# Kernel optimization log

Measured on AMD Instinct MI355X. Metric: run time of the kernel, lower is better.

## Reference

```python
import jax, jax.numpy as jnp
import numpy as np

EMBED_DIM = 1024
NUM_HEADS = 16
HEAD_DIM = EMBED_DIM // NUM_HEADS


def setup_inputs() -> dict:
    key = jax.random.key(0)
    ks = jax.random.split(key, 7)
    B, S, E = 8, 1024, EMBED_DIM
    # xavier-uniform-like scale for in_proj_weight [3E, E]
    bound_in = float(np.sqrt(6.0 / (3 * E + E)))
    bound_out = float(np.sqrt(6.0 / (E + E)))
    return {
        "q": jax.random.normal(ks[0], (B, S, E), jnp.float32),
        "k": jax.random.normal(ks[1], (B, S, E), jnp.float32),
        "v": jax.random.normal(ks[2], (B, S, E), jnp.float32),
        "in_proj_weight": jax.random.uniform(ks[3], (3 * E, E), jnp.float32, -bound_in, bound_in),
        "in_proj_bias": jnp.zeros((3 * E,), jnp.float32),
        "out_proj_weight": jax.random.uniform(ks[4], (E, E), jnp.float32, -bound_out, bound_out),
        "out_proj_bias": jnp.zeros((E,), jnp.float32),
    }


def reference(q, k, v, in_proj_weight, in_proj_bias, out_proj_weight, out_proj_bias):
    B, S, E = q.shape
    H, D = NUM_HEADS, HEAD_DIM
    w_q, w_k, w_v = jnp.split(in_proj_weight, 3, axis=0)
    b_q, b_k, b_v = jnp.split(in_proj_bias, 3, axis=0)
    # packed in-projection: linear(x, W, b) = x @ W.T + b
    qp = q @ w_q.T + b_q
    kp = k @ w_k.T + b_k
    vp = v @ w_v.T + b_v
    # [B, S, E] -> [B, H, S, D]
    qh = qp.reshape(B, S, H, D).transpose(0, 2, 1, 3)
    kh = kp.reshape(B, S, H, D).transpose(0, 2, 1, 3)
    vh = vp.reshape(B, S, H, D).transpose(0, 2, 1, 3)
    scale = D ** -0.5
    # explicit full attention in fp32 (matches original fp32 cast path)
    scores = jnp.einsum("bhqd,bhkd->bhqk", qh, kh) * scale
    attn = jax.nn.softmax(scores, axis=-1)
    ctx = jnp.einsum("bhqk,bhkd->bhqd", attn, vh)  # [B, H, S, D]
    ctx = ctx.transpose(0, 2, 1, 3).reshape(B, S, E)
    out = ctx @ out_proj_weight.T + out_proj_bias
    return out
```

## Files before the change

### kernel.cpp

```cpp
#include <hip/hip_runtime.h>
#include <stdint.h>

#define TOK 8192
#define EDIM 1024
#define NH 16
#define HD 64
#define SEQ 1024
#define BATCH 8

typedef short bf16x8 __attribute__((ext_vector_type(8)));
typedef short bf16x4 __attribute__((ext_vector_type(4)));
typedef float f32x4 __attribute__((ext_vector_type(4)));
typedef float f32x16 __attribute__((ext_vector_type(16)));
typedef unsigned int u32x2 __attribute__((ext_vector_type(2)));
typedef unsigned int u32x4 __attribute__((ext_vector_type(4)));

__device__ __forceinline__ short f2bf(float f) {
  union { float f; uint32_t u; } c; c.f = f;
  uint32_t u = c.u;
  u += 0x7FFFu + ((u >> 16) & 1u);
  return (short)(u >> 16);
}
__device__ __forceinline__ float bf2f(short h) {
  union { uint32_t u; float f; } c; c.u = ((uint32_t)(uint16_t)h) << 16;
  return c.f;
}
__device__ __forceinline__ uint32_t bfr(float f) {
  union { float f; uint32_t u; } c; c.f = f;
  return (c.u + 0x8000u) >> 16;
}
__device__ __forceinline__ uint32_t cvtpk(float lo, float hi_) {
  uint32_t r;
  asm("v_cvt_pk_bf16_f32 %0, %1, %2" : "=v"(r) : "v"(lo), "v"(hi_));
  return r;
}

#define GLDS16(ldsp, gp) __builtin_amdgcn_global_load_lds( \
    (__attribute__((address_space(1))) void*)(gp),          \
    (__attribute__((address_space(3))) void*)(ldsp), 16, 0, 0)

__global__ __launch_bounds__(256) void cast_all(
    const float* __restrict__ q, const float* __restrict__ k,
    const float* __restrict__ v, const float* __restrict__ wi,
    const float* __restrict__ wo, short* __restrict__ dst) {
  const size_t NTOK = (size_t)TOK * EDIM;
  const size_t NWI = 3u * EDIM * EDIM;
  size_t i = ((size_t)blockIdx.x * 256 + threadIdx.x) * 4;
  const float* src;
  if (i < NTOK) src = q + i;
  else if (i < 2 * NTOK) src = k + (i - NTOK);
  else if (i < 3 * NTOK) src = v + (i - 2 * NTOK);
  else if (i < 3 * NTOK + NWI) src = wi + (i - 3 * NTOK);
  else src = wo + (i - 3 * NTOK - NWI);
  float4 f = *(const float4*)src;
  bf16x4 o;
  o[0] = f2bf(f.x); o[1] = f2bf(f.y); o[2] = f2bf(f.z); o[3] = f2bf(f.w);
  *(bf16x4*)(dst + i) = o;
}

#define GEMM_TILE(KT, VMC, DOSTAGE)                                            \
  {                                                                            \
    asm volatile("s_waitcnt vmcnt(" VMC ")" ::: "memory");                     \
    __builtin_amdgcn_s_barrier();                                              \
    const int buf_ = (KT) & 3;                                                 \
    const short* Ab = lds + buf_ * 16384;                                      \
    const short* Bb = Ab + 8192;                                               \
    bf16x8 af[8], bv[4];                                                       \
    _Pragma("unroll")                                                          \
    for (int mi = 0; mi < 4; mi++)                                             \
      af[mi] = *(const bf16x8*)&Ab[(wrBase + mi * 16 + fr) * 32 + fg * 8];     \
    _Pragma("unroll")                                                          \
    for (int ni = 0; ni < 4; ni++)                                             \
      bv[ni] = *(const bf16x8*)&Bb[(wcBase + ni * 16 + fr) * 32 + fg * 8];     \
    if (DOSTAGE) {                                                             \
      char* d_ = (char*)lds + (((KT) + 3) & 3) * 32768 + t * 16;               \
      GLDS16(d_, aS + ((KT) + 3) * 32);                                        \
      GLDS16(d_ + 8192, aS + ((KT) + 3) * 32 + 128 * 1024);                    \
    }                                                                          \
    __builtin_amdgcn_s_setprio(1);                                             \
    _Pragma("unroll")                                                          \
    for (int mi = 0; mi < 4; mi++) {                                           \
      _Pragma("unroll")                                                        \
      for (int ni = 0; ni < 4; ni++)                                           \
        acc[mi][ni] = __builtin_amdgcn_mfma_f32_16x16x32_bf16(                 \
            af[mi], bv[ni], acc[mi][ni], 0, 0, 0);                             \
    }                                                                          \
    __builtin_amdgcn_s_setprio(0);                                             \
    _Pragma("unroll")                                                          \
    for (int mi = 4; mi < 8; mi++)                                             \
      af[mi] = *(const bf16x8*)&Ab[(wrBase + mi * 16 + fr) * 32 + fg * 8];     \
    if (DOSTAGE) {                                                             \
      char* d_ = (char*)lds + (((KT) + 3) & 3) * 32768 + 16384 + t * 16;       \
      GLDS16(d_, bS + ((KT) + 3) * 32);                                        \
      GLDS16(d_ + 8192, bS + ((KT) + 3) * 32 + 128 * 1024);                    \
    }                                                                          \
    __builtin_amdgcn_s_barrier();                                              \
    __builtin_amdgcn_s_setprio(1);                                             \
    _Pragma("unroll")                                                          \
    for (int mi = 4; mi < 8; mi++) {                                           \
      _Pragma("unroll")                                                        \
      for (int ni = 0; ni < 4; ni++)                                           \
        acc[mi][ni] = __builtin_amdgcn_mfma_f32_16x16x32_bf16(                 \
            af[mi], bv[ni], acc[mi][ni], 0, 0, 0);                             \
    }                                                                          \
    __builtin_amdgcn_s_setprio(0);                                             \
  }

template<int MODE>
__global__ __launch_bounds__(512, 1)
void gemm_bt8(const short* __restrict__ Abase, const short* __restrict__ Wbase,
              const float* __restrict__ biasBase, void* __restrict__ outv) {
  __shared__ short lds[65536];

  const int z = (MODE == 0) ? blockIdx.z : 0;
  const size_t NTOK = (size_t)TOK * EDIM;
  const short* A  = Abase + (size_t)z * NTOK;
  const short* Bw = Wbase + (size_t)z * EDIM * EDIM;
  const float* bias = biasBase + z * EDIM;

  const int t = threadIdx.x;
  const int l = t & 63, w = t >> 6;
  const int fr = l & 15, fg = l >> 4;
  const int wrBase = (w >> 2) * 128;
  const int wcBase = (w & 3) * 64;
  const int rowBase = blockIdx.x * 256;
  const int colBase = blockIdx.y * 256;

  f32x4 acc[8][4];
#pragma unroll
  for (int i = 0; i < 8; i++)
#pragma unroll
    for (int j = 0; j < 4; j++) acc[i][j] = (f32x4){0.f, 0.f, 0.f, 0.f};

  const short* aS = A  + (size_t)(rowBase + (t >> 2)) * EDIM + (t & 3) * 8;
  const short* bS = Bw + (size_t)(colBase + (t >> 2)) * EDIM + (t & 3) * 8;

#pragma unroll
  for (int s = 0; s < 3; s++) {
    char* d = (char*)lds + s * 32768 + t * 16;
    GLDS16(d,         aS + s * 32);
    GLDS16(d + 8192,  aS + s * 32 + 128 * 1024);
    GLDS16(d + 16384, bS + s * 32);
    GLDS16(d + 24576, bS + s * 32 + 128 * 1024);
  }

#pragma unroll 1
  for (int kt = 0; kt < 30; kt++) {
    GEMM_TILE(kt, "8", (kt <= 28));
  }
  GEMM_TILE(30, "4", false);
  GEMM_TILE(31, "0", false);

#pragma unroll
  for (int mi = 0; mi < 8; mi++)
#pragma unroll
    for (int ni = 0; ni < 4; ni++)
#pragma unroll
      for (int r = 0; r < 4; r++) {
        int grow = rowBase + wrBase + mi * 16 + fg * 4 + r;
        int gcol = colBase + wcBase + ni * 16 + fr;
        float v = acc[mi][ni][r] + bias[gcol];
        if (MODE == 0) {
          int b_ = grow >> 10, s_ = grow & 1023;
          int h_ = gcol >> 6,  d_ = gcol & 63;
          short* outp = (short*)outv + (size_t)z * NTOK;
          outp[((size_t)((b_ * NH + h_) * SEQ + s_) << 6) | d_] = f2bf(v);
        } else {
          ((float*)outv)[(size_t)grow * EDIM + gcol] = v;
        }
      }
}

__global__ __launch_bounds__(512)
void attn_fwd7(const short* __restrict__ proj, short* __restrict__ ctx) {
  __shared__ short lds[16384];

  const int t = threadIdx.x;
  const int l = t & 63, w = t >> 6;
  const int ln = l & 31, hi = l >> 5;

  const int n = blockIdx.x + 4 * (blockIdx.y + 16 * blockIdx.z);
  const int qt = (n >> 3) & 3;
  const int hl = (n & 7) | ((n >> 5) << 3);
  const int h = hl & 15, b = hl >> 4;

  const size_t NTOK = (size_t)TOK * EDIM;
  const size_t headOff = (size_t)(b * NH + h) * SEQ * HD;
  const short* Qp = proj + headOff;
  const short* Kp = proj + NTOK + headOff;
  const short* Vp = proj + 2 * NTOK + headOff;

  const int q0 = qt * 256;
  const int qrow = q0 + w * 32 + ln;

  const int kRow = t >> 3;
  const int kCol = ((t & 7) ^ (kRow & 7)) << 3;
  const int vd0  = w * 8;

  const float qscale = 0.18033688011112042f;
  bf16x8 bQ[4];
#pragma unroll
  for (int ds = 0; ds < 4; ds++) {
    bf16x8 v = *(const bf16x8*)(Qp + (size_t)qrow * HD + ds * 16 + hi * 8);
#pragma unroll
    for (int j = 0; j < 8; j++) v[j] = (short)bfr(bf2f(v[j]) * qscale);
    bQ[ds] = v;
  }

  float m_run = -3.0e38f;
  float l_acc[4] = {0.f, 0.f, 0.f, 0.f};
  f32x16 ot[2];
#pragma unroll
  for (int i = 0; i < 16; i++) { ot[0][i] = 0.f; ot[1][i] = 0.f; }

  {
    GLDS16((char*)lds + t * 16, Kp + (size_t)kRow * HD + kCol);
    bf16x8 v0 = *(const bf16x8*)(Vp + (size_t)l * HD + vd0);
    char* VtB = (char*)lds + 8192;
#pragma unroll
    for (int jj = 0; jj < 8; jj++) {
      int d = vd0 + jj;
      *(short*)(VtB + d * 128 + (((l >> 3) ^ (d & 7)) << 4) + (l & 7) * 2) = v0[jj];
    }
  }
  __syncthreads();

  for (int jt = 0; jt < SEQ / 64; jt++) {
    const int bufByte = (jt & 1) << 14;
    const int nb = bufByte ^ (1 << 14);
    const bool have_next = (jt + 1 < SEQ / 64);

    bf16x8 nv0;
    if (have_next) {
      const int kv1 = (jt + 1) * 64;
      GLDS16((char*)lds + nb + t * 16, Kp + (size_t)(kv1 + kRow) * HD + kCol);
      nv0 = *(const bf16x8*)(Vp + (size_t)(kv1 + l) * HD + vd0);
    }

    f32x16 sa[2];
#pragma unroll
    for (int i = 0; i < 16; i++) { sa[0][i] = 0.f; sa[1][i] = 0.f; }
    __builtin_amdgcn_s_setprio(1);
#pragma unroll
    for (int ds = 0; ds < 4; ds++) {
#pragma unroll
      for (int kvb = 0; kvb < 2; kvb++) {
        int kv = kvb * 32 + ln;
        bf16x8 aK = *(const bf16x8*)((const char*)lds + bufByte + kv * 128 +
                                     (((ds * 2 + hi) ^ (kv & 7)) << 4));
        sa[kvb] = __builtin_amdgcn_mfma_f32_32x32x16_bf16(aK, bQ[ds], sa[kvb], 0, 0, 0);
      }
    }
    __builtin_amdgcn_s_setprio(0);

    float tr[11];
#pragma unroll
    for (int j = 0; j < 10; j++) {
      float a = (3 * j + 0 < 16) ? sa[0][3 * j + 0] : sa[1][3 * j - 16];
      float b2 = (3 * j + 1 < 16) ? sa[0][3 * j + 1] : sa[1][3 * j - 15];
      float c = (3 * j + 2 < 16) ? sa[0][3 * j + 2] : sa[1][3 * j - 14];
      tr[j] = fmaxf(fmaxf(a, b2), c);
    }
    tr[10] = fmaxf(sa[1][14], sa[1][15]);
    float u0 = fmaxf(fmaxf(tr[0], tr[1]), tr[2]);
    float u1 = fmaxf(fmaxf(tr[3], tr[4]), tr[5]);
    float u2 = fmaxf(fmaxf(tr[6], tr[7]), tr[8]);
    float u3 = fmaxf(tr[9], tr[10]);
    float vmax = fmaxf(fmaxf(fmaxf(u0, u1), u2), u3);
    vmax = fmaxf(vmax, __shfl_xor(vmax, 32));

    int grow = !__all(vmax <= m_run + 8.0f);
    float alpha = 1.0f;
    if (grow) {
      float m_new = fmaxf(m_run, vmax);
      alpha = exp2f(m_run - m_new);
      m_run = m_new;
    }
    float ps[4] = {0.f, 0.f, 0.f, 0.f};
#pragma unroll
    for (int i = 0; i < 16; i++) {
      float p0 = exp2f(sa[0][i] - m_run);
      float p1 = exp2f(sa[1][i] - m_run);
      sa[0][i] = p0; sa[1][i] = p1;
      ps[i & 3] += p0 + p1;
    }
#pragma unroll
    for (int j = 0; j < 4; j++) l_acc[j] = l_acc[j] * alpha + ps[j];

    bf16x8 pa[4];
#pragma unroll
    for (int ks = 0; ks < 4; ks++) {
      const int kvb = ks >> 1, hf = (ks & 1) * 8;
      uint32_t A1 = cvtpk(sa[kvb][hf + 0], sa[kvb][hf + 1]);
      uint32_t A2 = cvtpk(sa[kvb][hf + 2], sa[kvb][hf + 3]);
      uint32_t B1 = cvtpk(sa[kvb][hf + 4], sa[kvb][hf + 5]);
      uint32_t B2 = cvtpk(sa[kvb][hf + 6], sa[kvb][hf + 7]);
      u32x4 wds;
#if __has_builtin(__builtin_amdgcn_permlane32_swap)
      u32x2 r13 = __builtin_amdgcn_permlane32_swap(A1, B1, false, false);
      u32x2 r24 = __builtin_amdgcn_permlane32_swap(A2, B2, false, false);
      wds[0] = r13[0]; wds[2] = r13[1];
      wds[1] = r24[0]; wds[3] = r24[1];
#else
      uint32_t send1 = hi ? A1 : B1;
      uint32_t send2 = hi ? A2 : B2;
      uint32_t recv1 = (uint32_t)__shfl_xor((int)send1, 32);
      uint32_t recv2 = (uint32_t)__shfl_xor((int)send2, 32);
      wds[0] = hi ? recv1 : A1;
      wds[1] = hi ? recv2 : A2;
      wds[2] = hi ? B1 : recv1;
      wds[3] = hi ? B2 : recv2;
#endif
      pa[ks] = __builtin_bit_cast(bf16x8, wds);
    }

    if (grow) {
#pragma unroll
      for (int i = 0; i < 16; i++) { ot[0][i] *= alpha; ot[1][i] *= alpha; }
    }
    const char* VtB = (const char*)lds + bufByte + 8192;
    __builtin_amdgcn_s_setprio(1);
#pragma unroll
    for (int ks = 0; ks < 4; ks++) {
#pragma unroll
      for (int dblk = 0; dblk < 2; dblk++) {
        int d = dblk * 32 + ln;
        bf16x8 aV = *(const bf16x8*)(VtB + d * 128 + (((ks * 2 + hi) ^ (d & 7)) << 4));
        ot[dblk] = __builtin_amdgcn_mfma_f32_32x32x16_bf16(aV, pa[ks], ot[dblk], 0, 0, 0);
      }
    }
    __builtin_amdgcn_s_setprio(0);

    if (have_next) {
      char* VtN = (char*)lds + nb + 8192;
#pragma unroll
      for (int jj = 0; jj < 8; jj++) {
        int d = vd0 + jj;
        *(short*)(VtN + d * 128 + (((l >> 3) ^ (d & 7)) << 4) + (l & 7) * 2) = nv0[jj];
      }
    }

    __syncthreads();
  }

  float l_run = (l_acc[0] + l_acc[1]) + (l_acc[2] + l_acc[3]);
  l_run += __shfl_xor(l_run, 32);
  float rl = 1.0f / l_run;

#pragma unroll
  for (int dblk = 0; dblk < 2; dblk++)
#pragma unroll
    for (int r = 0; r < 16; r++) {
      int d = dblk * 32 + (r & 3) + 8 * (r >> 2) + 4 * hi;
      int qrl = w * 32 + ln;
      int byteoff = qrl * 128 + (((d >> 3) ^ (qrl & 7)) << 4) + (d & 7) * 2;
      *(short*)((char*)lds + byteoff) = (short)bfr(ot[dblk][r] * rl);
    }
  __syncthreads();
#pragma unroll
  for (int i = 0; i < 4; i++) {
    int chunk = t * 4 + i;
    int row = chunk >> 3, c8 = chunk & 7;
    bf16x8 vv = *(const bf16x8*)((const char*)lds + row * 128 + ((c8 ^ (row & 7)) << 4));
    *(bf16x8*)(ctx + (size_t)(b * SEQ + q0 + row) * EDIM + h * HD + c8 * 8) = vv;
  }
}

extern "C" void kernel_launch(void* const* d_in, const int* in_sizes, int n_in,
                              void* d_out, int out_size, void* d_ws, size_t ws_size,
                              hipStream_t stream) {
  const float* q  = (const float*)d_in[0];
  const float* k  = (const float*)d_in[1];
  const float* v  = (const float*)d_in[2];
  const float* wi = (const float*)d_in[3];
  const float* bi = (const float*)d_in[4];
  const float* wo = (const float*)d_in[5];
  const float* bo = (const float*)d_in[6];
  float* out = (float*)d_out;

  short* ws = (short*)d_ws;
  const size_t NTOK = (size_t)TOK * EDIM;
  short* qkv_bf   = ws;
  short* w_in_bf  = qkv_bf + 3 * NTOK;
  short* w_out_bf = w_in_bf + 3 * (size_t)EDIM * EDIM;
  short* proj_bf  = w_out_bf + (size_t)EDIM * EDIM;
  short* ctx_bf   = qkv_bf;

  const size_t totalCast = 3 * NTOK + 3 * (size_t)EDIM * EDIM + (size_t)EDIM * EDIM;
  cast_all<<<dim3((unsigned)(totalCast / 4 / 256)), 256, 0, stream>>>(q, k, v, wi, wo, qkv_bf);

  gemm_bt8<0><<<dim3(TOK / 256, EDIM / 256, 3), 512, 0, stream>>>(qkv_bf, w_in_bf, bi, proj_bf);
  attn_fwd7<<<dim3(SEQ / 256, NH, BATCH), 512, 0, stream>>>(proj_bf, ctx_bf);
  gemm_bt8<1><<<dim3(TOK / 256, EDIM / 256, 1), 512, 0, stream>>>(ctx_bf, w_out_bf, bo, out);
}
```

Before: 190.2 us.

## Software-pipeline QK^T of next tile with softmax of current tile in attention

Restructures the attention loop so the QK^T MFMAs for tile jt+1 are computed while the softmax exponentials and bf16 packing for tile jt run, with score registers ping-ponging between two sets. K/V staging in LDS goes from a double buffer to a four-slot ring (64 KB), with global loads issued two tiles ahead. The aim is to overlap MFMA work with VALU/transcendental work and hide load latency. The costs are more registers and twice the LDS, which may lower occupancy.

```diff
diff --git a/kernel.cpp b/kernel.cpp
--- a/kernel.cpp
+++ b/kernel.cpp
@@ -172,8 +172,8 @@
 }
 
 __global__ __launch_bounds__(512)
-void attn_fwd7(const short* __restrict__ proj, short* __restrict__ ctx) {
-  __shared__ short lds[16384];
+void attn_fwd8(const short* __restrict__ proj, short* __restrict__ ctx) {
+  __shared__ short lds[32768];
 
   const int t = threadIdx.x;
   const int l = t & 63, w = t >> 6;
@@ -213,139 +213,186 @@
 #pragma unroll
   for (int i = 0; i < 16; i++) { ot[0][i] = 0.f; ot[1][i] = 0.f; }
 
+  f32x16 saA[2], saB[2];
+  bf16x8 nvA, nvB;
+
   {
-    GLDS16((char*)lds + t * 16, Kp + (size_t)kRow * HD + kCol);
-    bf16x8 v0 = *(const bf16x8*)(Vp + (size_t)l * HD + vd0);
-    char* VtB = (char*)lds + 8192;
+    GLDS16((char*)lds + t * 16,         Kp + (size_t)kRow * HD + kCol);
+    GLDS16((char*)lds + 16384 + t * 16, Kp + (size_t)(64 + kRow) * HD + kCol);
+    bf16x8 v0r = *(const bf16x8*)(Vp + (size_t)l * HD + vd0);
+    nvB = *(const bf16x8*)(Vp + (size_t)(64 + l) * HD + vd0);
+    char* Vt0 = (char*)lds + 8192;
 #pragma unroll
     for (int jj = 0; jj < 8; jj++) {
       int d = vd0 + jj;
-      *(short*)(VtB + d * 128 + (((l >> 3) ^ (d & 7)) << 4) + (l & 7) * 2) = v0[jj];
+      *(short*)(Vt0 + d * 128 + (((l >> 3) ^ (d & 7)) << 4) + (l & 7) * 2) = v0r[jj];
     }
-  }
-  __syncthreads();
-
-  for (int jt = 0; jt < SEQ / 64; jt++) {
-    const int bufByte = (jt & 1) << 14;
-    const int nb = bufByte ^ (1 << 14);
-    const bool have_next = (jt + 1 < SEQ / 64);
-
-    bf16x8 nv0;
-    if (have_next) {
-      const int kv1 = (jt + 1) * 64;
-      GLDS16((char*)lds + nb + t * 16, Kp + (size_t)(kv1 + kRow) * HD + kCol);
-      nv0 = *(const bf16x8*)(Vp + (size_t)(kv1 + l) * HD + vd0);
+    __syncthreads();
+#pragma unroll
+    for (int kvb = 0; kvb < 2; kvb++) {
+      f32x16 s = {};
+#pragma unroll
+      for (int ds = 0; ds < 4; ds++) {
+        int kv = kvb * 32 + ln;
+        bf16x8 aK = *(const bf16x8*)((const char*)lds + kv * 128 +
+                                     (((ds * 2 + hi) ^ (kv & 7)) << 4));
+        s = __builtin_amdgcn_mfma_f32_32x32x16_bf16(aK, bQ[ds], s, 0, 0, 0);
+      }
+      saA[kvb] = s;
     }
-
-    f32x16 sa[2];
-#pragma unroll
-    for (int i = 0; i < 16; i++) { sa[0][i] = 0.f; sa[1][i] = 0.f; }
-    __builtin_amdgcn_s_setprio(1);
-#pragma unroll
-    for (int ds = 0; ds < 4; ds++) {
-#pragma unroll
-      for (int kvb = 0; kvb < 2; kvb++) {
-        int kv = kvb * 32 + ln;
-        bf16x8 aK = *(const bf16x8*)((const char*)lds + bufByte + kv * 128 +
-                                     (((ds * 2 + hi) ^ (kv & 7)) << 4));
-        sa[kvb] = __builtin_amdgcn_mfma_f32_32x32x16_bf16(aK, bQ[ds], sa[kvb], 0, 0, 0);
-      }
-    }
-    __builtin_amdgcn_s_setprio(0);
-
-    float tr[11];
-#pragma unroll
-    for (int j = 0; j < 10; j++) {
-      float a = (3 * j + 0 < 16) ? sa[0][3 * j + 0] : sa[1][3 * j - 16];
-      float b2 = (3 * j + 1 < 16) ? sa[0][3 * j + 1] : sa[1][3 * j - 15];
-      float c = (3 * j + 2 < 16) ? sa[0][3 * j + 2] : sa[1][3 * j - 14];
-      tr[j] = fmaxf(fmaxf(a, b2), c);
-    }
-    tr[10] = fmaxf(sa[1][14], sa[1][15]);
-    float u0 = fmaxf(fmaxf(tr[0], tr[1]), tr[2]);
-    float u1 = fmaxf(fmaxf(tr[3], tr[4]), tr[5]);
-    float u2 = fmaxf(fmaxf(tr[6], tr[7]), tr[8]);
-    float u3 = fmaxf(tr[9], tr[10]);
-    float vmax = fmaxf(fmaxf(fmaxf(u0, u1), u2), u3);
-    vmax = fmaxf(vmax, __shfl_xor(vmax, 32));
-
-    int grow = !__all(vmax <= m_run + 8.0f);
-    float alpha = 1.0f;
-    if (grow) {
-      float m_new = fmaxf(m_run, vmax);
-      alpha = exp2f(m_run - m_new);
-      m_run = m_new;
-    }
-    float ps[4] = {0.f, 0.f, 0.f, 0.f};
-#pragma unroll
-    for (int i = 0; i < 16; i++) {
-      float p0 = exp2f(sa[0][i] - m_run);
-      float p1 = exp2f(sa[1][i] - m_run);
-      sa[0][i] = p0; sa[1][i] = p1;
-      ps[i & 3] += p0 + p1;
-    }
-#pragma unroll
-    for (int j = 0; j < 4; j++) l_acc[j] = l_acc[j] * alpha + ps[j];
-
-    bf16x8 pa[4];
-#pragma unroll
-    for (int ks = 0; ks < 4; ks++) {
-      const int kvb = ks >> 1, hf = (ks & 1) * 8;
-      uint32_t A1 = cvtpk(sa[kvb][hf + 0], sa[kvb][hf + 1]);
-      uint32_t A2 = cvtpk(sa[kvb][hf + 2], sa[kvb][hf + 3]);
-      uint32_t B1 = cvtpk(sa[kvb][hf + 4], sa[kvb][hf + 5]);
-      uint32_t B2 = cvtpk(sa[kvb][hf + 6], sa[kvb][hf + 7]);
-      u32x4 wds;
-#if __has_builtin(__builtin_amdgcn_permlane32_swap)
-      u32x2 r13 = __builtin_amdgcn_permlane32_swap(A1, B1, false, false);
-      u32x2 r24 = __builtin_amdgcn_permlane32_swap(A2, B2, false, false);
-      wds[0] = r13[0]; wds[2] = r13[1];
-      wds[1] = r24[0]; wds[3] = r24[1];
-#else
-      uint32_t send1 = hi ? A1 : B1;
-      uint32_t send2 = hi ? A2 : B2;
-      uint32_t recv1 = (uint32_t)__shfl_xor((int)send1, 32);
-      uint32_t recv2 = (uint32_t)__shfl_xor((int)send2, 32);
-      wds[0] = hi ? recv1 : A1;
-      wds[1] = hi ? recv2 : A2;
-      wds[2] = hi ? B1 : recv1;
-      wds[3] = hi ? B2 : recv2;
-#endif
-      pa[ks] = __builtin_bit_cast(bf16x8, wds);
-    }
-
-    if (grow) {
-#pragma unroll
-      for (int i = 0; i < 16; i++) { ot[0][i] *= alpha; ot[1][i] *= alpha; }
-    }
-    const char* VtB = (const char*)lds + bufByte + 8192;
-    __builtin_amdgcn_s_setprio(1);
-#pragma unroll
-    for (int ks = 0; ks < 4; ks++) {
-#pragma unroll
-      for (int dblk = 0; dblk < 2; dblk++) {
-        int d = dblk * 32 + ln;
-        bf16x8 aV = *(const bf16x8*)(VtB + d * 128 + (((ks * 2 + hi) ^ (d & 7)) << 4));
-        ot[dblk] = __builtin_amdgcn_mfma_f32_32x32x16_bf16(aV, pa[ks], ot[dblk], 0, 0, 0);
-      }
-    }
-    __builtin_amdgcn_s_setprio(0);
-
-    if (have_next) {
-      char* VtN = (char*)lds + nb + 8192;
-#pragma unroll
-      for (int jj = 0; jj < 8; jj++) {
-        int d = vd0 + jj;
-        *(short*)(VtN + d * 128 + (((l >> 3) ^ (d & 7)) << 4) + (l & 7) * 2) = nv0[jj];
-      }
-    }
-
-    __syncthreads();
-  }
+  }
+
+#define ATTN_BODY(JT, SACUR, SANEXT, NVOLD, NVNEW)                             \
+  {                                                                            \
+    const int jt_ = (JT);                                                      \
+    __syncthreads();             \
+    if (jt_ + 2 < 16) {                       \
+      const int kv2 = (jt_ + 2) * 64;                                          \
+      GLDS16((char*)lds + ((jt_ + 2) & 3) * 16384 + t * 16,                    \
+             Kp + (size_t)(kv2 + kRow) * HD + kCol);                           \
+      NVNEW = *(const bf16x8*)(Vp + (size_t)(kv2 + l) * HD + vd0);             \
+    }                                                                          \
+                                                      \
+    float tr[11];                                                              \
+    _Pragma("unroll")                                                          \
+    for (int j = 0; j < 10; j++) {                                             \
+      float a_ = (3 * j + 0 < 16) ? SACUR[0][3 * j + 0] : SACUR[1][3 * j - 16];\
+      float b_ = (3 * j + 1 < 16) ? SACUR[0][3 * j + 1] : SACUR[1][3 * j - 15];\
+      float c_ = (3 * j + 2 < 16) ? SACUR[0][3 * j + 2] : SACUR[1][3 * j - 14];\
+      tr[j] = fmaxf(fmaxf(a_, b_), c_);                                        \
+    }                                                                          \
+    tr[10] = fmaxf(SACUR[1][14], SACUR[1][15]);                                \
+    float u0 = fmaxf(fmaxf(tr[0], tr[1]), tr[2]);                              \
+    float u1 = fmaxf(fmaxf(tr[3], tr[4]), tr[5]);                              \
+    float u2 = fmaxf(fmaxf(tr[6], tr[7]), tr[8]);                              \
+    float vmax = fmaxf(fmaxf(fmaxf(u0, u1), u2), fmaxf(tr[9], tr[10]));        \
+    vmax = fmaxf(vmax, __shfl_xor(vmax, 32));                                  \
+    int grow = !__all(vmax <= m_run + 8.0f);                                   \
+    float alpha = 1.0f;                                                        \
+    if (grow) {                                                                \
+      float m_new = fmaxf(m_run, vmax);                                        \
+      alpha = exp2f(m_run - m_new);                                            \
+      m_run = m_new;                                                           \
+    }                                                                          \
+    float ps[4] = {0.f, 0.f, 0.f, 0.f};                                        \
+    bf16x8 pa[4];                                                              \
+                 \
+    {                                                                          \
+      float p[16];                                                             \
+      _Pragma("unroll")                                                        \
+      for (int i = 0; i < 16; i++) {                                           \
+        p[i] = exp2f(SACUR[0][i] - m_run);                                     \
+        ps[i & 3] += p[i];                                                     \
+      }                                                                        \
+      _Pragma("unroll")                                                        \
+      for (int ks = 0; ks < 2; ks++) {                                         \
+        const int hf = ks * 8;                                                 \
+        uint32_t A1 = cvtpk(p[hf + 0], p[hf + 1]);                             \
+        uint32_t A2 = cvtpk(p[hf + 2], p[hf + 3]);                             \
+        uint32_t B1 = cvtpk(p[hf + 4], p[hf + 5]);                             \
+        uint32_t B2 = cvtpk(p[hf + 6], p[hf + 7]);                             \
+        u32x4 wds;                                                             \
+        u32x2 r13 = __builtin_amdgcn_permlane32_swap(A1, B1, false, false);    \
+        u32x2 r24 = __builtin_amdgcn_permlane32_swap(A2, B2, false, false);    \
+        wds[0] = r13[0]; wds[2] = r13[1];                                      \
+        wds[1] = r24[0]; wds[3] = r24[1];                                      \
+        pa[ks] = __builtin_bit_cast(bf16x8, wds);                              \
+      }                                                                        \
+    }                                                                          \
+    if (jt_ + 1 < 16) {      \
+      f32x16 s = {};                                                           \
+      _Pragma("unroll")                                                        \
+      for (int ds = 0; ds < 4; ds++) {                                         \
+        int kv = ln;                                                           \
+        bf16x8 aK = *(const bf16x8*)((const char*)lds +                        \
+                     ((jt_ + 1) & 3) * 16384 + kv * 128 +                      \
+                     (((ds * 2 + hi) ^ (kv & 7)) << 4));                       \
+        s = __builtin_amdgcn_mfma_f32_32x32x16_bf16(aK, bQ[ds], s, 0, 0, 0);   \
+      }                                                                        \
+      SANEXT[0] = s;                                                           \
+    }                                                                          \
+                                                                   \
+    {                                                                          \
+      float p[16];                                                             \
+      _Pragma("unroll")                                                        \
+      for (int i = 0; i < 16; i++) {                                           \
+        p[i] = exp2f(SACUR[1][i] - m_run);                                     \
+        ps[i & 3] += p[i];                                                     \
+      }                                                                        \
+      _Pragma("unroll")                                                        \
+      for (int ks = 0; ks < 2; ks++) {                                         \
+        const int hf = ks * 8;                                                 \
+        uint32_t A1 = cvtpk(p[hf + 0], p[hf + 1]);                             \
+        uint32_t A2 = cvtpk(p[hf + 2], p[hf + 3]);                             \
+        uint32_t B1 = cvtpk(p[hf + 4], p[hf + 5]);                             \
+        uint32_t B2 = cvtpk(p[hf + 6], p[hf + 7]);                             \
+        u32x4 wds;                                                             \
+        u32x2 r13 = __builtin_amdgcn_permlane32_swap(A1, B1, false, false);    \
+        u32x2 r24 = __builtin_amdgcn_permlane32_swap(A2, B2, false, false);    \
+        wds[0] = r13[0]; wds[2] = r13[1];                                      \
+        wds[1] = r24[0]; wds[3] = r24[1];                                      \
+        pa[2 + ks] = __builtin_bit_cast(bf16x8, wds);                          \
+      }                                                                        \
+    }                                                                          \
+    if (jt_ + 1 < 16) {                                    \
+      f32x16 s = {};                                                           \
+      _Pragma("unroll")                                                        \
+      for (int ds = 0; ds < 4; ds++) {                                         \
+        int kv = 32 + ln;                                                      \
+        bf16x8 aK = *(const bf16x8*)((const char*)lds +                        \
+                     ((jt_ + 1) & 3) * 16384 + kv * 128 +                      \
+                     (((ds * 2 + hi) ^ (kv & 7)) << 4));                       \
+        s = __builtin_amdgcn_mfma_f32_32x32x16_bf16(aK, bQ[ds], s, 0, 0, 0);   \
+      }                                                                        \
+      SANEXT[1] = s;                                                           \
+    }                                                                          \
+    _Pragma("unroll")                                                          \
+    for (int j = 0; j < 4; j++) l_acc[j] = l_acc[j] * alpha + ps[j];           \
+    if (grow) {                                                                \
+      _Pragma("unroll")                                                        \
+      for (int i = 0; i < 16; i++) { ot[0][i] *= alpha; ot[1][i] *= alpha; }   \
+    }                                                                          \
+                                                                   \
+    {                                                                          \
+      const char* VtB = (const char*)lds + (jt_ & 3) * 16384 + 8192;           \
+      __builtin_amdgcn_s_setprio(1);                                           \
+      _Pragma("unroll")                                                        \
+      for (int ks = 0; ks < 4; ks++) {                                         \
+        _Pragma("unroll")                                                      \
+        for (int dblk = 0; dblk < 2; dblk++) {                                 \
+          int d = dblk * 32 + ln;                                              \
+          bf16x8 aV = *(const bf16x8*)(VtB + d * 128 +                         \
+                       (((ks * 2 + hi) ^ (d & 7)) << 4));                      \
+          ot[dblk] = __builtin_amdgcn_mfma_f32_32x32x16_bf16(                  \
+              aV, pa[ks], ot[dblk], 0, 0, 0);                                  \
+        }                                                                      \
+      }                                                                        \
+      __builtin_amdgcn_s_setprio(0);                                           \
+    }                                                                          \
+               \
+    if (jt_ + 1 < 16) {                                                        \
+      char* VtN = (char*)lds + ((jt_ + 1) & 3) * 16384 + 8192;                 \
+      _Pragma("unroll")                                                        \
+      for (int jj = 0; jj < 8; jj++) {                                         \
+        int d = vd0 + jj;                                                      \
+        *(short*)(VtN + d * 128 + (((l >> 3) ^ (d & 7)) << 4) +                \
+                  (l & 7) * 2) = NVOLD[jj];                                    \
+      }                                                                        \
+    }                                                                          \
+  }
+
+#pragma unroll 1
+  for (int j2 = 0; j2 < 8; j2++) {
+    ATTN_BODY(2 * j2,     saA, saB, nvB, nvA);
+    ATTN_BODY(2 * j2 + 1, saB, saA, nvA, nvB);
+  }
+#undef ATTN_BODY
 
   float l_run = (l_acc[0] + l_acc[1]) + (l_acc[2] + l_acc[3]);
   l_run += __shfl_xor(l_run, 32);
   float rl = 1.0f / l_run;
+
+  __syncthreads();
 
 #pragma unroll
   for (int dblk = 0; dblk < 2; dblk++)
@@ -390,6 +437,6 @@
   cast_all<<<dim3((unsigned)(totalCast / 4 / 256)), 256, 0, stream>>>(q, k, v, wi, wo, qkv_bf);
 
   gemm_bt8<0><<<dim3(TOK / 256, EDIM / 256, 3), 512, 0, stream>>>(qkv_bf, w_in_bf, bi, proj_bf);
-  attn_fwd7<<<dim3(SEQ / 256, NH, BATCH), 512, 0, stream>>>(proj_bf, ctx_bf);
+  attn_fwd8<<<dim3(SEQ / 256, NH, BATCH), 512, 0, stream>>>(proj_bf, ctx_bf);
   gemm_bt8<1><<<dim3(TOK / 256, EDIM / 256, 1), 512, 0, stream>>>(ctx_bf, w_out_bf, bo, out);
 }
```

Result: no change. 189.2 us (-0.5%).
